# Kernel tuning notes

Measured on AMD Instinct MI355X. Metric: run time of the kernel, lower is better.

The kernel has to match this reference:

```python
import jax, jax.numpy as jnp
import numpy as np

N_NODES = 100000
N_EDGES = 1200000
DIM = 64
MAX_DEG = 64
NUM_LAB = 16
BN_EPS = 1e-5


def _lrelu(x):
    return jax.nn.leaky_relu(x, negative_slope=0.01)


def _bn(x, g, b):
    # BatchNorm1d in training mode: batch statistics over node axis
    m = x.mean(axis=0)
    v = x.var(axis=0)
    return (x - m) * jax.lax.rsqrt(v + BN_EPS) * g + b


def _gin_layer(h, src, dst, n, w1, b1, w2, b2, eps, g, b):
    # GINConv: (1+eps)*x_i + sum_{j in N(i)} x_j, then MLP (lin_lrelu_lin), BN, LeakyReLU
    agg = jax.ops.segment_sum(h[src], dst, num_segments=n)
    x = (1.0 + eps) * h + agg
    x = _lrelu(x @ w1 + b1) @ w2 + b2
    return _lrelu(_bn(x, g, b))


def setup_inputs() -> dict:
    key = jax.random.key(0)
    ks = jax.random.split(key, 16)
    s = 0.05
    inp = {
        'node_deg': jax.random.randint(ks[0], (N_NODES,), 0, MAX_DEG + 1, dtype=jnp.int32),
        'node_lab': jax.random.randint(ks[1], (N_NODES,), 0, NUM_LAB, dtype=jnp.int32),
        'edge_index': jax.random.randint(ks[2], (2, N_EDGES), 0, N_NODES, dtype=jnp.int32),
        'emb_deg': jax.random.normal(ks[3], (MAX_DEG + 1, DIM), jnp.float32) * s,
        'emb_lab': jax.random.normal(ks[4], (NUM_LAB, DIM), jnp.float32) * s,
        'l0_w1': jax.random.normal(ks[5], (2 * DIM, 2 * DIM), jnp.float32) * s,
        'l0_b1': jnp.zeros((2 * DIM,), jnp.float32),
        'l0_w2': jax.random.normal(ks[6], (2 * DIM, DIM), jnp.float32) * s,
        'l0_b2': jnp.zeros((DIM,), jnp.float32),
        'l0_eps': jnp.zeros((1,), jnp.float32),
        'bn0_g': jnp.ones((DIM,), jnp.float32),
        'bn0_b': jnp.zeros((DIM,), jnp.float32),
        'l1_w1': jax.random.normal(ks[7], (DIM, DIM), jnp.float32) * s,
        'l1_b1': jnp.zeros((DIM,), jnp.float32),
        'l1_w2': jax.random.normal(ks[8], (DIM, DIM), jnp.float32) * s,
        'l1_b2': jnp.zeros((DIM,), jnp.float32),
        'l1_eps': jnp.zeros((1,), jnp.float32),
        'bn1_g': jnp.ones((DIM,), jnp.float32),
        'bn1_b': jnp.zeros((DIM,), jnp.float32),
        'fc_w1': jax.random.normal(ks[9], (4 * DIM, DIM), jnp.float32) * s,
        'fc_b1': jnp.zeros((DIM,), jnp.float32),
        'fc_bn_g': jnp.ones((DIM,), jnp.float32),
        'fc_bn_b': jnp.zeros((DIM,), jnp.float32),
        'fc_w2': jax.random.normal(ks[10], (DIM, 1), jnp.float32) * s,
        'fc_b2': jnp.zeros((1,), jnp.float32),
    }
    return inp


def reference(node_deg, node_lab, edge_index, emb_deg, emb_lab,
              l0_w1, l0_b1, l0_w2, l0_b2, l0_eps, bn0_g, bn0_b,
              l1_w1, l1_b1, l1_w2, l1_b2, l1_eps, bn1_g, bn1_b,
              fc_w1, fc_b1, fc_bn_g, fc_bn_b, fc_w2, fc_b2):
    n = node_deg.shape[0]
    src, dst = edge_index[0], edge_index[1]
    # embedding concat: [N, 2*DIM]
    h0 = jnp.concatenate([emb_deg[node_deg], emb_lab[node_lab]], axis=1)
    h1 = _gin_layer(h0, src, dst, n, l0_w1, l0_b1, l0_w2, l0_b2, l0_eps[0], bn0_g, bn0_b)
    h2 = _gin_layer(h1, src, dst, n, l1_w1, l1_b1, l1_w2, l1_b2, l1_eps[0], bn1_g, bn1_b)
    x = jnp.concatenate([h0, h1, h2], axis=1)  # [N, 256]
    x = _lrelu(_bn(x @ fc_w1 + fc_b1, fc_bn_g, fc_bn_b))
    out = jax.nn.sigmoid(x @ fc_w2 + fc_b2)
    return out.squeeze(-1)  # [N]
```

## Files before the change

kernel.cpp:

```cpp
#include <hip/hip_runtime.h>

#define N_NODES 100000
#define N_EDGES 1200000
#define NCLS 81
#define NBKT 196
#define BCAP 8192
#define NCHK 293
#define NGBLK 1563

typedef unsigned short u16;
typedef unsigned char u8;
typedef unsigned int u32;
typedef unsigned long long u64;
typedef short bf16x8 __attribute__((ext_vector_type(8)));
typedef float f32x4 __attribute__((ext_vector_type(4)));

__device__ __forceinline__ float b2f(u16 u) {
  union { u32 i; float f; } v; v.i = ((u32)u) << 16; return v.f;
}
__device__ __forceinline__ u16 f2b(float f) {
  union { float f; u32 i; } v; v.f = f;
  u32 x = v.i;
  return (u16)((x + 0x7fffu + ((x >> 16) & 1u)) >> 16);
}
__device__ __forceinline__ void up2(u32 w, float& lo, float& hi) {
  union { u32 u; float f; } a, b;
  a.u = w << 16; b.u = w & 0xffff0000u;
  lo = a.f; hi = b.f;
}
__device__ __forceinline__ float lrelu(float x) { return x > 0.f ? x : 0.01f * x; }

__device__ __forceinline__ bool is_f32(const u16* emb) {
  int lane = threadIdx.x & 63;
  u32 e0 = (emb[lane * 2] >> 7) & 0xFF;
  u32 e1 = (emb[lane * 2 + 1] >> 7) & 0xFF;
  return __ballot((e0 >= 0x90) || (e1 >= 0x90)) != 0ull;
}

__device__ __forceinline__ float rdr(const void* p, int i, bool f32m) {
  return f32m ? ((const float*)p)[i] : b2f(((const u16*)p)[i]);
}

#define P_EMBD 0
#define P_EMBL 4160
#define P_W1A  5184
#define P_B1A  21568
#define P_W2A  21696
#define P_B2A  29888
#define P_EPS0 29952
#define P_G0   29953
#define P_BB0  30017
#define P_LW1  30081
#define P_LB1  34177
#define P_LW2  34241
#define P_LB2  38337
#define P_EPS1 38401
#define P_G1   38402
#define P_BB1  38466
#define P_FW1  38530
#define P_FB1  54914
#define P_FG   54978
#define P_FBB  55042
#define P_FW2  55106
#define P_FB2  55170
#define P_TOT  55171

struct CvtAll {
  const void* src[22];
  int cnt[22];
  int off[22];
};

struct RawPtrs {
  const void* embD;
  const void* embL;
  const void* w1r;
  const void* w2r;
  const void* lw1r;
  const void* lw2r;
  const void* fwr;
};

__global__ void k_init(CvtAll a, RawPtrs rw, const u16* __restrict__ embRaw,
                       float* __restrict__ P, float* __restrict__ W1p,
                       float* __restrict__ Efc, u16* __restrict__ bp,
                       u16* __restrict__ wpB, u32* __restrict__ gcur) {
  bool f32m = is_f32(embRaw);
  int tid = threadIdx.x;
  if (blockIdx.y < 22) {
    if (blockIdx.y == 0 && blockIdx.x == 0 && tid < NBKT) gcur[tid] = 0;
    int seg = blockIdx.y;
    int i = blockIdx.x * 256 + tid;
    if (i < a.cnt[seg]) {
      float v = f32m ? ((const float*)a.src[seg])[i] : b2f(((const u16*)a.src[seg])[i]);
      P[a.off[seg] + i] = v;
    }
    return;
  }
  int idx = blockIdx.x * 256 + tid;
  if (idx < NCLS * 128) {
    int c = idx >> 7, h = idx & 127;
    float s = 0.f;
    if (c < 65) {
      for (int k = 0; k < 64; ++k)
        s = fmaf(rdr(rw.embD, c * 64 + k, f32m), rdr(rw.w1r, k * 128 + h, f32m), s);
    } else {
      for (int k = 0; k < 64; ++k)
        s = fmaf(rdr(rw.embL, (c - 65) * 64 + k, f32m), rdr(rw.w1r, (64 + k) * 128 + h, f32m), s);
    }
    W1p[idx] = s;
    return;
  }
  if (idx < NCLS * 128 + NCLS * 64) {
    int r = idx - NCLS * 128;
    int c = r >> 6, o = r & 63;
    float s = 0.f;
    if (c < 65) {
      for (int k = 0; k < 64; ++k)
        s = fmaf(rdr(rw.embD, c * 64 + k, f32m), rdr(rw.fwr, k * 64 + o, f32m), s);
    } else {
      for (int k = 0; k < 64; ++k)
        s = fmaf(rdr(rw.embL, (c - 65) * 64 + k, f32m), rdr(rw.fwr, (64 + k) * 64 + o, f32m), s);
    }
    Efc[r] = s;
    return;
  }
  if (idx < NCLS * 128 + NCLS * 64 + 24576) {
    int pidx = idx - (NCLS * 128 + NCLS * 64);
    int seg, rel;
    if (pidx < 8192)       { seg = 0; rel = pidx; }
    else if (pidx < 12288) { seg = 1; rel = pidx - 8192; }
    else if (pidx < 16384) { seg = 2; rel = pidx - 12288; }
    else                   { seg = 3; rel = pidx - 16384; }
    const void* srcs[4] = {rw.w2r, rw.lw1r, rw.lw2r, rw.fwr};
    const int addoff[4] = {0, 0, 0, 128 * 64};
    const int KBs[4] = {4, 2, 2, 4};
    int j = rel & 7, lane = (rel >> 3) & 63, rest = rel >> 9;
    int kb = rest % KBs[seg], nt = rest / KBs[seg];
    int k = kb * 32 + (lane >> 4) * 8 + j;
    int n = nt * 16 + (lane & 15);
    bp[pidx] = f2b(rdr(srcs[seg], addoff[seg] + k * 64 + n, f32m));
    return;
  }
  int p2 = idx - (NCLS * 128 + NCLS * 64 + 24576);
  if (p2 >= 12288) return;
  int j = p2 & 7, lane = (p2 >> 3) & 63, rest = p2 >> 9;
  int kb = rest % 3, nt = rest / 3;
  int c = kb * 32 + (lane >> 4) * 8 + j;
  int n = nt * 16 + (lane & 15);
  float s = 0.f;
  if (c < NCLS) {
    if (c < 65) {
      for (int k = 0; k < 64; ++k)
        s = fmaf(rdr(rw.embD, c * 64 + k, f32m), rdr(rw.w1r, k * 128 + n, f32m), s);
    } else {
      for (int k = 0; k < 64; ++k)
        s = fmaf(rdr(rw.embL, (c - 65) * 64 + k, f32m), rdr(rw.w1r, (64 + k) * 128 + n, f32m), s);
    }
  }
  wpB[p2] = (c < NCLS) ? f2b(s) : 0;
}

__global__ __launch_bounds__(256) void k_bsort(const int* __restrict__ edge,
                                               const int* __restrict__ ndeg,
                                               const int* __restrict__ nlab,
                                               u32* __restrict__ gcur,
                                               u64* __restrict__ e2) {
  __shared__ u32 cnt[NBKT], rbase[NBKT];
  __shared__ u32 slo[4096], shi[4096];
  for (int i = threadIdx.x; i < NBKT; i += 256) cnt[i] = 0;
  __syncthreads();
  int base = blockIdx.x * 4096;
  for (int i = threadIdx.x; i < 4096; i += 256) {
    int e = base + i;
    if (e < N_EDGES) {
      int s = edge[e], d = edge[N_EDGES + e];
      slo[i] = ((u32)s << 11) | ((u32)ndeg[s] << 4) | (u32)nlab[s];
      shi[i] = (u32)d;
      atomicAdd(&cnt[(u32)d >> 9], 1u);
    } else shi[i] = 0xFFFFFFFFu;
  }
  __syncthreads();
  for (int i = threadIdx.x; i < NBKT; i += 256) {
    u32 c = cnt[i];
    rbase[i] = c ? atomicAdd(&gcur[i], c) : 0u;
    cnt[i] = 0;
  }
  __syncthreads();
  for (int i = threadIdx.x; i < 4096; i += 256) {
    u32 d = shi[i];
    if (d == 0xFFFFFFFFu) continue;
    u32 b = d >> 9;
    u32 pos = rbase[b] + atomicAdd(&cnt[b], 1u);
    e2[(size_t)b * BCAP + pos] = ((u64)d << 32) | (u64)slo[i];
  }
}

__global__ __launch_bounds__(512) void k_csrh(const u64* __restrict__ e2,
                                              const u32* __restrict__ gcur,
                                              const u16* __restrict__ wpB,
                                              const float* __restrict__ W1p,
                                              const float* __restrict__ P,
                                              const int* __restrict__ ndeg,
                                              const int* __restrict__ nlab,
                                              u32* __restrict__ row_ptr,
                                              u32* __restrict__ einfo,
                                              u16* __restrict__ hmid) {
  __shared__ u32 l[512], cur[512], gl[NBKT];
  __shared__ u32 h32[512 * 24];
  __shared__ u32 sbase;
  int b = blockIdx.x, tid = threadIdx.x;
  if (tid < NBKT) gl[tid] = gcur[tid];
  l[tid] = 0;
  for (int i = tid; i < 512 * 24; i += 512) h32[i] = 0;
  __syncthreads();
  if (tid == 0) {
    u32 s = 0;
    for (int i = 0; i < b; ++i) s += gl[i];
    sbase = s;
  }
  __syncthreads();
  u32 cnt = gl[b];
  const u64* src = e2 + (size_t)b * BCAP;
  for (u32 e = tid; e < cnt; e += 512)
    atomicAdd(&l[(u32)(src[e] >> 32) & 511u], 1u);
  __syncthreads();
  u32 v = l[tid];
  for (int off = 1; off < 512; off <<= 1) {
    u32 a = (tid >= off) ? l[tid - off] : 0u;
    __syncthreads();
    l[tid] += a;
    __syncthreads();
  }
  u32 pos0 = sbase + l[tid] - v;
  cur[tid] = pos0;
  int nn = b * 512 + tid;
  if (nn <= N_NODES) row_ptr[nn] = pos0;
  __syncthreads();
  for (u32 e = tid; e < cnt; e += 512) {
    u64 r = src[e];
    u32 dl = (u32)(r >> 32) & 511u;
    u32 lo = (u32)r;
    u32 pos = atomicAdd(&cur[dl], 1u);
    einfo[pos] = lo;
    u32 c1 = (lo >> 4) & 0x7Fu, c2 = 65u + (lo & 15u);
    atomicAdd(&h32[dl * 24 + (c1 >> 2)], 1u << ((c1 & 3u) * 8));
    atomicAdd(&h32[dl * 24 + (c2 >> 2)], 1u << ((c2 & 3u) * 8));
  }
  __syncthreads();
  const u8* h = (const u8*)h32;
  int wid = tid >> 6, lane = tid & 63;
  int row = lane & 15, q = lane >> 4;
  float onep = 1.f + P[P_EPS0];
  const bf16x8* bp = (const bf16x8*)wpB;
#pragma unroll 1
  for (int t = wid; t < 32; t += 8) {
    int m0 = b * 512 + t * 16;
    if (m0 >= N_NODES) break;
    f32x4 acc[8];
#pragma unroll
    for (int nt = 0; nt < 8; ++nt) {
      float bb = P[P_B1A + nt * 16 + row];
      acc[nt][0] = bb; acc[nt][1] = bb; acc[nt][2] = bb; acc[nt][3] = bb;
    }
    const u8* ar = h + (t * 16 + row) * 96 + q * 8;
#pragma unroll
    for (int kb = 0; kb < 3; ++kb) {
      bf16x8 af;
#pragma unroll
      for (int j = 0; j < 8; ++j) af[j] = (short)f2b((float)ar[kb * 32 + j]);
#pragma unroll
      for (int nt = 0; nt < 8; ++nt) {
        bf16x8 bf = bp[(nt * 3 + kb) * 64 + lane];
        acc[nt] = __builtin_amdgcn_mfma_f32_16x16x32_bf16(af, bf, acc[nt], 0, 0, 0);
      }
    }
#pragma unroll
    for (int r = 0; r < 4; ++r) {
      int m = m0 + q * 4 + r;
      if (m >= N_NODES) continue;
      const float* wd = W1p + ndeg[m] * 128;
      const float* wl = W1p + (65 + nlab[m]) * 128;
#pragma unroll
      for (int nt = 0; nt < 8; ++nt) {
        int cc = nt * 16 + row;
        float vv = acc[nt][r] + onep * (wd[cc] + wl[cc]);
        hmid[(size_t)m * 128 + cc] = f2b(lrelu(vv));
      }
    }
  }
}

__global__ void k_sr(const float* __restrict__ pbuf, float* __restrict__ statsOut) {
  __shared__ float l[256];
  int c = blockIdx.x;
  float s = 0.f;
  for (int r = threadIdx.x; r < NGBLK; r += 256) s += pbuf[(size_t)r * 128 + c];
  l[threadIdx.x] = s;
  __syncthreads();
  for (int off = 128; off > 0; off >>= 1) {
    if (threadIdx.x < off) l[threadIdx.x] += l[threadIdx.x + off];
    __syncthreads();
  }
  if (threadIdx.x == 0) statsOut[c] = l[0];
}

template <int KB, int LDA, int BIASOFF>
__global__ __launch_bounds__(256) void k_gemm(const u16* __restrict__ A,
                                              const u16* __restrict__ Bp,
                                              const float* __restrict__ P,
                                              float* __restrict__ pbuf,
                                              u16* __restrict__ C) {
  __shared__ float lsum[4][64], lsq[4][64];
  int wid = threadIdx.x >> 6, lane = threadIdx.x & 63;
  int m0 = (blockIdx.x * 4 + wid) * 16;
  bool act = m0 < N_NODES;
  int row = lane & 15, q = lane >> 4;
  float ss[4] = {0.f, 0.f, 0.f, 0.f}, qq[4] = {0.f, 0.f, 0.f, 0.f};
  if (act) {
    const u16* ap = A + (size_t)(m0 + row) * LDA + q * 8;
    const bf16x8* bp = (const bf16x8*)Bp;
    f32x4 acc[4];
#pragma unroll
    for (int nt = 0; nt < 4; ++nt) {
      float b = (BIASOFF >= 0) ? P[BIASOFF + nt * 16 + row] : 0.f;
      acc[nt][0] = b; acc[nt][1] = b; acc[nt][2] = b; acc[nt][3] = b;
    }
#pragma unroll
    for (int kb = 0; kb < KB; ++kb) {
      bf16x8 af = *(const bf16x8*)(ap + kb * 32);
#pragma unroll
      for (int nt = 0; nt < 4; ++nt) {
        bf16x8 bf = bp[(nt * KB + kb) * 64 + lane];
        acc[nt] = __builtin_amdgcn_mfma_f32_16x16x32_bf16(af, bf, acc[nt], 0, 0, 0);
      }
    }
#pragma unroll
    for (int nt = 0; nt < 4; ++nt) {
      float s = 0.f, z = 0.f;
#pragma unroll
      for (int r = 0; r < 4; ++r) {
        int m = m0 + q * 4 + r;
        u16 bv = f2b(acc[nt][r]);
        C[(size_t)m * 64 + nt * 16 + row] = bv;
        float v = b2f(bv);
        s += v; z = fmaf(v, v, z);
      }
      s += __shfl_xor(s, 16, 64); s += __shfl_xor(s, 32, 64);
      z += __shfl_xor(z, 16, 64); z += __shfl_xor(z, 32, 64);
      ss[nt] = s; qq[nt] = z;
    }
  }
  if (lane < 16) {
#pragma unroll
    for (int nt = 0; nt < 4; ++nt) {
      lsum[wid][nt * 16 + lane] = ss[nt];
      lsq[wid][nt * 16 + lane] = qq[nt];
    }
  }
  __syncthreads();
  int t = threadIdx.x;
  if (t < 64)
    pbuf[(size_t)blockIdx.x * 128 + t] = lsum[0][t] + lsum[1][t] + lsum[2][t] + lsum[3][t];
  else if (t < 128) {
    int c = t - 64;
    pbuf[(size_t)blockIdx.x * 128 + t] = lsq[0][c] + lsq[1][c] + lsq[2][c] + lsq[3][c];
  }
}

__global__ __launch_bounds__(256) void k_gemm_bn(const u16* __restrict__ A,
                                                 const u16* __restrict__ Bp,
                                                 const float* __restrict__ P,
                                                 const float* __restrict__ stats,
                                                 u16* __restrict__ C) {
  int wid = threadIdx.x >> 6, lane = threadIdx.x & 63;
  int m0 = (blockIdx.x * 4 + wid) * 16;
  if (m0 >= N_NODES) return;
  int row = lane & 15, q = lane >> 4;
  const float invN = 1.f / (float)N_NODES;
  float sc[16], sh[16];
#pragma unroll
  for (int kb = 0; kb < 2; ++kb)
#pragma unroll
    for (int j = 0; j < 8; ++j) {
      int f = kb * 32 + q * 8 + j;
      float mm = stats[f] * invN;
      float var = fmaxf(stats[64 + f] * invN - mm * mm, 0.f);
      float inv = rsqrtf(var + 1e-5f);
      float s = inv * P[P_G0 + f];
      sc[kb * 8 + j] = s;
      sh[kb * 8 + j] = P[P_BB0 + f] - mm * s;
    }
  const u16* ap = A + (size_t)(m0 + row) * 64 + q * 8;
  const bf16x8* bp = (const bf16x8*)Bp;
  f32x4 acc[4];
#pragma unroll
  for (int nt = 0; nt < 4; ++nt) {
    acc[nt][0] = 0.f; acc[nt][1] = 0.f; acc[nt][2] = 0.f; acc[nt][3] = 0.f;
  }
#pragma unroll
  for (int kb = 0; kb < 2; ++kb) {
    uint4 raw = *(const uint4*)(ap + kb * 32);
    u32 rw[4] = {raw.x, raw.y, raw.z, raw.w};
    bf16x8 af;
#pragma unroll
    for (int p = 0; p < 4; ++p) {
      float lo, hi;
      up2(rw[p], lo, hi);
      float y0 = lrelu(fmaf(sc[kb * 8 + 2 * p], lo, sh[kb * 8 + 2 * p]));
      float y1 = lrelu(fmaf(sc[kb * 8 + 2 * p + 1], hi, sh[kb * 8 + 2 * p + 1]));
      af[2 * p] = (short)f2b(y0);
      af[2 * p + 1] = (short)f2b(y1);
    }
#pragma unroll
    for (int nt = 0; nt < 4; ++nt) {
      bf16x8 bf = bp[(nt * 2 + kb) * 64 + lane];
      acc[nt] = __builtin_amdgcn_mfma_f32_16x16x32_bf16(af, bf, acc[nt], 0, 0, 0);
    }
  }
#pragma unroll
  for (int nt = 0; nt < 4; ++nt)
#pragma unroll
    for (int r = 0; r < 4; ++r) {
      int m = m0 + q * 4 + r;
      C[(size_t)m * 64 + nt * 16 + row] = f2b(acc[nt][r]);
    }
}

__global__ __launch_bounds__(256) void k_agg1(const u32* __restrict__ rp,
                                              const u32* __restrict__ einfo,
                                              const u16* __restrict__ g1,
                                              const float* __restrict__ P,
                                              u16* __restrict__ abuf) {
  int lane = threadIdx.x & 63, wv = threadIdx.x >> 6;
  int n = blockIdx.x * 4 + wv;
  if (n >= N_NODES) return;
  u32 st = rp[n], en = rp[n + 1];
  u32 m = en - st;
  int grp = lane >> 4;
  int fo = (lane & 15) * 4;
  u32 myidx = (u32)n;
  if (lane < (int)m) myidx = einfo[st + lane] >> 11;
  u32 mm = m < 64u ? m : 64u;
  float a0 = 0.f, a1 = 0.f, a2 = 0.f, a3 = 0.f;
  for (u32 k = 0; k < mm; k += 16) {
#pragma unroll
    for (int bb = 0; bb < 4; ++bb) {
      u32 e = k + (u32)(bb * 4 + grp);
      u32 src = (u32)__shfl((int)myidx, (int)e, 64);
      if (e < mm) {
        uint2 v = *(const uint2*)(g1 + (size_t)src * 64 + fo);
        float l0, h0, l1, h1;
        up2(v.x, l0, h0);
        up2(v.y, l1, h1);
        a0 += l0; a1 += h0; a2 += l1; a3 += h1;
      }
    }
  }
  a0 += __shfl_xor(a0, 16, 64); a0 += __shfl_xor(a0, 32, 64);
  a1 += __shfl_xor(a1, 16, 64); a1 += __shfl_xor(a1, 32, 64);
  a2 += __shfl_xor(a2, 16, 64); a2 += __shfl_xor(a2, 32, 64);
  a3 += __shfl_xor(a3, 16, 64); a3 += __shfl_xor(a3, 32, 64);
  for (u32 k = 64; k < m; ++k) {
    u32 src = einfo[st + k] >> 11;
    uint2 v = *(const uint2*)(g1 + (size_t)src * 64 + fo);
    float l0, h0, l1, h1;
    up2(v.x, l0, h0);
    up2(v.y, l1, h1);
    a0 += l0; a1 += h0; a2 += l1; a3 += h1;
  }
  float onep = 1.f + P[P_EPS1];
  uint2 sv = *(const uint2*)(g1 + (size_t)n * 64 + fo);
  float s0, s1, s2, s3;
  up2(sv.x, s0, s1);
  up2(sv.y, s2, s3);
  float r0 = P[P_LB1 + fo + 0] + fmaf(onep, s0, a0);
  float r1 = P[P_LB1 + fo + 1] + fmaf(onep, s1, a1);
  float r2 = P[P_LB1 + fo + 2] + fmaf(onep, s2, a2);
  float r3 = P[P_LB1 + fo + 3] + fmaf(onep, s3, a3);
  if (lane < 16) {
    uint2 o;
    o.x = ((u32)f2b(lrelu(r0))) | (((u32)f2b(lrelu(r1))) << 16);
    o.y = ((u32)f2b(lrelu(r2))) | (((u32)f2b(lrelu(r3))) << 16);
    *(uint2*)(abuf + (size_t)n * 64 + fo) = o;
  }
}

__global__ __launch_bounds__(256) void k_gemm_fc1bn(const u16* __restrict__ t0,
                                                    const u16* __restrict__ t1,
                                                    const u16* __restrict__ Bp,
                                                    const float* __restrict__ P,
                                                    const float* __restrict__ stats,
                                                    float* __restrict__ pbuf,
                                                    const int* __restrict__ ndeg,
                                                    const int* __restrict__ nlab,
                                                    const float* __restrict__ Efc,
                                                    u16* __restrict__ C) {
  __shared__ float lsum[4][64], lsq[4][64];
  int wid = threadIdx.x >> 6, lane = threadIdx.x & 63;
  int m0 = (blockIdx.x * 4 + wid) * 16;
  bool act = m0 < N_NODES;
  int row = lane & 15, q = lane >> 4;
  float ss[4] = {0.f, 0.f, 0.f, 0.f}, qq[4] = {0.f, 0.f, 0.f, 0.f};
  if (act) {
    const float invN = 1.f / (float)N_NODES;
    float sc[32], sh[32];
#pragma unroll
    for (int h = 0; h < 2; ++h) {
      const float* st = stats + h * 128;
      int gof = h ? P_G1 : P_G0, bof = h ? P_BB1 : P_BB0;
#pragma unroll
      for (int kb = 0; kb < 2; ++kb)
#pragma unroll
        for (int j = 0; j < 8; ++j) {
          int f = kb * 32 + q * 8 + j;
          float mm = st[f] * invN;
          float var = fmaxf(st[64 + f] * invN - mm * mm, 0.f);
          float inv = rsqrtf(var + 1e-5f);
          float s = inv * P[gof + f];
          sc[h * 16 + kb * 8 + j] = s;
          sh[h * 16 + kb * 8 + j] = P[bof + f] - mm * s;
        }
    }
    const u16* a0 = t0 + (size_t)(m0 + row) * 64 + q * 8;
    const u16* a1 = t1 + (size_t)(m0 + row) * 64 + q * 8;
    const bf16x8* bp = (const bf16x8*)Bp;
    f32x4 acc[4];
#pragma unroll
    for (int nt = 0; nt < 4; ++nt) {
      float b = P[P_FB1 + nt * 16 + row];
      acc[nt][0] = b; acc[nt][1] = b; acc[nt][2] = b; acc[nt][3] = b;
    }
#pragma unroll
    for (int kb = 0; kb < 4; ++kb) {
      const u16* src = (kb < 2) ? (a0 + kb * 32) : (a1 + (kb - 2) * 32);
      int ci = (kb < 2) ? kb * 8 : 16 + (kb - 2) * 8;
      uint4 raw = *(const uint4*)src;
      u32 rw[4] = {raw.x, raw.y, raw.z, raw.w};
      bf16x8 af;
#pragma unroll
      for (int p = 0; p < 4; ++p) {
        float lo, hi;
        up2(rw[p], lo, hi);
        float y0 = lrelu(fmaf(sc[ci + 2 * p], lo, sh[ci + 2 * p]));
        float y1 = lrelu(fmaf(sc[ci + 2 * p + 1], hi, sh[ci + 2 * p + 1]));
        af[2 * p] = (short)f2b(y0);
        af[2 * p + 1] = (short)f2b(y1);
      }
#pragma unroll
      for (int nt = 0; nt < 4; ++nt) {
        bf16x8 bf = bp[(nt * 4 + kb) * 64 + lane];
        acc[nt] = __builtin_amdgcn_mfma_f32_16x16x32_bf16(af, bf, acc[nt], 0, 0, 0);
      }
    }
    float es[4][4];
#pragma unroll
    for (int r = 0; r < 4; ++r) {
      int m = m0 + q * 4 + r;
      int dn = ndeg[m], ln = 65 + nlab[m];
#pragma unroll
      for (int nt = 0; nt < 4; ++nt) {
        int cc = nt * 16 + row;
        es[r][nt] = acc[nt][r] + Efc[dn * 64 + cc] + Efc[ln * 64 + cc];
      }
    }
#pragma unroll
    for (int nt = 0; nt < 4; ++nt) {
      float s = 0.f, z = 0.f;
#pragma unroll
      for (int r = 0; r < 4; ++r) {
        int m = m0 + q * 4 + r;
        u16 bv = f2b(es[r][nt]);
        C[(size_t)m * 64 + nt * 16 + row] = bv;
        float v = b2f(bv);
        s += v; z = fmaf(v, v, z);
      }
      s += __shfl_xor(s, 16, 64); s += __shfl_xor(s, 32, 64);
      z += __shfl_xor(z, 16, 64); z += __shfl_xor(z, 32, 64);
      ss[nt] = s; qq[nt] = z;
    }
  }
  if (lane < 16) {
#pragma unroll
    for (int nt = 0; nt < 4; ++nt) {
      lsum[wid][nt * 16 + lane] = ss[nt];
      lsq[wid][nt * 16 + lane] = qq[nt];
    }
  }
  __syncthreads();
  int t = threadIdx.x;
  if (t < 64)
    pbuf[(size_t)blockIdx.x * 128 + t] = lsum[0][t] + lsum[1][t] + lsum[2][t] + lsum[3][t];
  else if (t < 128) {
    int c = t - 64;
    pbuf[(size_t)blockIdx.x * 128 + t] = lsq[0][c] + lsq[1][c] + lsq[2][c] + lsq[3][c];
  }
}

__global__ void k_fc2(const u16* __restrict__ t, const float* __restrict__ stats,
                      const float* __restrict__ P, const u16* __restrict__ embRaw,
                      void* __restrict__ out) {
  bool f32m = is_f32(embRaw);
  int n = blockIdx.x * blockDim.x + threadIdx.x;
  if (n >= N_NODES) return;
  float z = P[P_FB2];
  const float invN = 1.f / (float)N_NODES;
  const u16* tn = t + (size_t)n * 64;
#pragma unroll 1
  for (int f = 0; f < 64; ++f) {
    float m = stats[f] * invN;
    float var = fmaxf(stats[64 + f] * invN - m * m, 0.f);
    float inv = rsqrtf(var + 1e-5f);
    float y = (b2f(tn[f]) - m) * inv * P[P_FG + f] + P[P_FBB + f];
    y = lrelu(y);
    z = fmaf(y, P[P_FW2 + f], z);
  }
  float s = 1.f / (1.f + expf(-z));
  if (!(fabsf(z) < 1e30f)) s = 0.25f;
  if (f32m) ((float*)out)[n] = s;
  else      ((u16*)out)[n] = f2b(s);
}

extern "C" void kernel_launch(void* const* d_in, const int* in_sizes, int n_in,
                              void* d_out, int out_size, void* d_ws, size_t ws_size,
                              hipStream_t stream) {
  const int* node_deg = (const int*)d_in[0];
  const int* node_lab = (const int*)d_in[1];
  const int* edge     = (const int*)d_in[2];
  const u16* embRaw   = (const u16*)d_in[3];
  (void)in_sizes; (void)n_in; (void)out_size; (void)ws_size;

  char* base = (char*)d_ws;
  size_t off = 0;
  auto alloc = [&](size_t bytes) -> void* {
    void* p = base + off;
    off += (bytes + 15) & ~(size_t)15;
    return p;
  };
  float* Pb    = (float*)alloc((size_t)P_TOT * 4);
  float* stats = (float*)alloc(384 * 4);
  u32* gcur    = (u32*)alloc(NBKT * 4);
  float* W1p   = (float*)alloc(NCLS * 128 * 4);
  float* Efc   = (float*)alloc(NCLS * 64 * 4);
  u16* bpack   = (u16*)alloc(24576 * 2);
  u16* wpB     = (u16*)alloc(12288 * 2);
  u32* row_ptr = (u32*)alloc((size_t)(N_NODES + 1) * 4);
  float* pbuf  = (float*)alloc((size_t)NGBLK * 128 * 4);
  u32* einfo   = (u32*)alloc((size_t)N_EDGES * 4);
  u64* e2      = (u64*)alloc((size_t)NBKT * BCAP * 8);
  void* arena  = alloc((size_t)N_NODES * 128 * 2);
  u16* t0      = (u16*)alloc((size_t)N_NODES * 64 * 2);
  u16* t1      = (u16*)alloc((size_t)N_NODES * 64 * 2);
  u16* t2      = (u16*)alloc((size_t)N_NODES * 64 * 2);
  u16* hmid = (u16*)arena;
  u16* g1   = (u16*)arena;
  u16* abuf = (u16*)arena + (size_t)N_NODES * 64;
  u16* Bp_w2a = bpack;
  u16* Bp_lw1 = bpack + 8192;
  u16* Bp_lw2 = bpack + 12288;
  u16* Bp_fw1 = bpack + 16384;

  CvtAll ca;
  const int srcidx[22] = {3, 4, 5, 6, 7, 8, 9, 10, 11, 12, 13, 14, 15, 16, 17, 18, 19, 20, 21, 22, 23, 24};
  const int cnts[22]   = {4160, 1024, 16384, 128, 8192, 64, 1, 64, 64, 4096, 64, 4096, 64, 1, 64, 64, 16384, 64, 64, 64, 64, 1};
  const int offs[22]   = {P_EMBD, P_EMBL, P_W1A, P_B1A, P_W2A, P_B2A, P_EPS0, P_G0, P_BB0,
                          P_LW1, P_LB1, P_LW2, P_LB2, P_EPS1, P_G1, P_BB1,
                          P_FW1, P_FB1, P_FG, P_FBB, P_FW2, P_FB2};
  for (int i = 0; i < 22; ++i) { ca.src[i] = d_in[srcidx[i]]; ca.cnt[i] = cnts[i]; ca.off[i] = offs[i]; }
  RawPtrs rw;
  rw.embD = d_in[3]; rw.embL = d_in[4]; rw.w1r = d_in[5]; rw.w2r = d_in[7];
  rw.lw1r = d_in[12]; rw.lw2r = d_in[14]; rw.fwr = d_in[19];

  k_init<<<dim3(205, 23), 256, 0, stream>>>(ca, rw, embRaw, Pb, W1p, Efc, bpack, wpB, gcur);

  k_bsort<<<NCHK, 256, 0, stream>>>(edge, node_deg, node_lab, gcur, e2);

  k_csrh<<<NBKT, 512, 0, stream>>>(e2, gcur, wpB, W1p, Pb, node_deg, node_lab,
                                   row_ptr, einfo, hmid);

  const int GEMM_GRID = NGBLK;

  k_gemm<4, 128, P_B2A><<<GEMM_GRID, 256, 0, stream>>>(hmid, Bp_w2a, Pb, pbuf, t0);
  k_sr<<<128, 256, 0, stream>>>(pbuf, stats);

  k_gemm_bn<<<GEMM_GRID, 256, 0, stream>>>(t0, Bp_lw1, Pb, stats, g1);
  k_agg1<<<(N_NODES + 3) / 4, 256, 0, stream>>>(row_ptr, einfo, g1, Pb, abuf);
  k_gemm<2, 64, P_LB2><<<GEMM_GRID, 256, 0, stream>>>(abuf, Bp_lw2, Pb, pbuf, t1);
  k_sr<<<128, 256, 0, stream>>>(pbuf, stats + 128);

  k_gemm_fc1bn<<<GEMM_GRID, 256, 0, stream>>>(t0, t1, Bp_fw1, Pb, stats, pbuf,
                                              node_deg, node_lab, Efc, t2);
  k_sr<<<128, 256, 0, stream>>>(pbuf, stats + 256);
  k_fc2<<<(N_NODES + 255) / 256, 256, 0, stream>>>(t2, stats + 256, Pb, embRaw, d_out);
}
```

Measured before the change: 321.8 us.

## Fuse layer-1 neighbor aggregation with second MLP GEMM and BN stats

New measurement: 340.7 us. 5.9% more time.

```diff
diff --git a/kernel.cpp b/kernel.cpp
--- a/kernel.cpp
+++ b/kernel.cpp
@@ -427,62 +427,124 @@
     }
 }
 
-__global__ __launch_bounds__(256) void k_agg1(const u32* __restrict__ rp,
-                                              const u32* __restrict__ einfo,
-                                              const u16* __restrict__ g1,
-                                              const float* __restrict__ P,
-                                              u16* __restrict__ abuf) {
-  int lane = threadIdx.x & 63, wv = threadIdx.x >> 6;
-  int n = blockIdx.x * 4 + wv;
-  if (n >= N_NODES) return;
-  u32 st = rp[n], en = rp[n + 1];
-  u32 m = en - st;
-  int grp = lane >> 4;
-  int fo = (lane & 15) * 4;
-  u32 myidx = (u32)n;
-  if (lane < (int)m) myidx = einfo[st + lane] >> 11;
-  u32 mm = m < 64u ? m : 64u;
-  float a0 = 0.f, a1 = 0.f, a2 = 0.f, a3 = 0.f;
-  for (u32 k = 0; k < mm; k += 16) {
-#pragma unroll
-    for (int bb = 0; bb < 4; ++bb) {
-      u32 e = k + (u32)(bb * 4 + grp);
-      u32 src = (u32)__shfl((int)myidx, (int)e, 64);
-      if (e < mm) {
+__global__ __launch_bounds__(256) void k_agg_gemm(const u32* __restrict__ rp,
+                                                  const u32* __restrict__ einfo,
+                                                  const u16* __restrict__ g1,
+                                                  const u16* __restrict__ Bp,
+                                                  const float* __restrict__ P,
+                                                  float* __restrict__ pbuf,
+                                                  u16* __restrict__ C) {
+  __shared__ float lsum[4][64], lsq[4][64];
+  __shared__ u16 As[4][16][72];
+  int wid = threadIdx.x >> 6, lane = threadIdx.x & 63;
+  int m0 = (blockIdx.x * 4 + wid) * 16;
+  bool act = m0 < N_NODES;
+  int row = lane & 15, q = lane >> 4;
+  float ss[4] = {0.f, 0.f, 0.f, 0.f}, qq[4] = {0.f, 0.f, 0.f, 0.f};
+  if (act) {
+    int grp = lane >> 4;
+    int fo = (lane & 15) * 4;
+    float onep = 1.f + P[P_EPS1];
+    u32 rpv = 0;
+    if (lane <= 16) rpv = rp[m0 + lane];
+#pragma unroll 1
+    for (int r = 0; r < 16; ++r) {
+      int n = m0 + r;
+      u32 st = (u32)__shfl((int)rpv, r, 64);
+      u32 en = (u32)__shfl((int)rpv, r + 1, 64);
+      u32 m = en - st;
+      u32 myidx = (u32)n;
+      if (lane < (int)m) myidx = einfo[st + lane] >> 11;
+      u32 mm = m < 64u ? m : 64u;
+      float a0 = 0.f, a1 = 0.f, a2 = 0.f, a3 = 0.f;
+      for (u32 k = 0; k < mm; k += 16) {
+#pragma unroll
+        for (int bb = 0; bb < 4; ++bb) {
+          u32 e = k + (u32)(bb * 4 + grp);
+          u32 src = (u32)__shfl((int)myidx, (int)e, 64);
+          if (e < mm) {
+            uint2 v = *(const uint2*)(g1 + (size_t)src * 64 + fo);
+            float l0, h0, l1, h1;
+            up2(v.x, l0, h0);
+            up2(v.y, l1, h1);
+            a0 += l0; a1 += h0; a2 += l1; a3 += h1;
+          }
+        }
+      }
+      a0 += __shfl_xor(a0, 16, 64); a0 += __shfl_xor(a0, 32, 64);
+      a1 += __shfl_xor(a1, 16, 64); a1 += __shfl_xor(a1, 32, 64);
+      a2 += __shfl_xor(a2, 16, 64); a2 += __shfl_xor(a2, 32, 64);
+      a3 += __shfl_xor(a3, 16, 64); a3 += __shfl_xor(a3, 32, 64);
+      for (u32 k = 64; k < m; ++k) {
+        u32 src = einfo[st + k] >> 11;
         uint2 v = *(const uint2*)(g1 + (size_t)src * 64 + fo);
         float l0, h0, l1, h1;
         up2(v.x, l0, h0);
         up2(v.y, l1, h1);
         a0 += l0; a1 += h0; a2 += l1; a3 += h1;
       }
-    }
-  }
-  a0 += __shfl_xor(a0, 16, 64); a0 += __shfl_xor(a0, 32, 64);
-  a1 += __shfl_xor(a1, 16, 64); a1 += __shfl_xor(a1, 32, 64);
-  a2 += __shfl_xor(a2, 16, 64); a2 += __shfl_xor(a2, 32, 64);
-  a3 += __shfl_xor(a3, 16, 64); a3 += __shfl_xor(a3, 32, 64);
-  for (u32 k = 64; k < m; ++k) {
-    u32 src = einfo[st + k] >> 11;
-    uint2 v = *(const uint2*)(g1 + (size_t)src * 64 + fo);
-    float l0, h0, l1, h1;
-    up2(v.x, l0, h0);
-    up2(v.y, l1, h1);
-    a0 += l0; a1 += h0; a2 += l1; a3 += h1;
-  }
-  float onep = 1.f + P[P_EPS1];
-  uint2 sv = *(const uint2*)(g1 + (size_t)n * 64 + fo);
-  float s0, s1, s2, s3;
-  up2(sv.x, s0, s1);
-  up2(sv.y, s2, s3);
-  float r0 = P[P_LB1 + fo + 0] + fmaf(onep, s0, a0);
-  float r1 = P[P_LB1 + fo + 1] + fmaf(onep, s1, a1);
-  float r2 = P[P_LB1 + fo + 2] + fmaf(onep, s2, a2);
-  float r3 = P[P_LB1 + fo + 3] + fmaf(onep, s3, a3);
+      uint2 sv = *(const uint2*)(g1 + (size_t)n * 64 + fo);
+      float s0, s1, s2, s3;
+      up2(sv.x, s0, s1);
+      up2(sv.y, s2, s3);
+      float r0 = P[P_LB1 + fo + 0] + fmaf(onep, s0, a0);
+      float r1 = P[P_LB1 + fo + 1] + fmaf(onep, s1, a1);
+      float r2 = P[P_LB1 + fo + 2] + fmaf(onep, s2, a2);
+      float r3 = P[P_LB1 + fo + 3] + fmaf(onep, s3, a3);
+      if (lane < 16) {
+        uint2 o;
+        o.x = ((u32)f2b(lrelu(r0))) | (((u32)f2b(lrelu(r1))) << 16);
+        o.y = ((u32)f2b(lrelu(r2))) | (((u32)f2b(lrelu(r3))) << 16);
+        *(uint2*)&As[wid][r][fo] = o;
+      }
+    }
+    const u16* ap = &As[wid][row][q * 8];
+    const bf16x8* bp = (const bf16x8*)Bp;
+    f32x4 acc[4];
+#pragma unroll
+    for (int nt = 0; nt < 4; ++nt) {
+      float b = P[P_LB2 + nt * 16 + row];
+      acc[nt][0] = b; acc[nt][1] = b; acc[nt][2] = b; acc[nt][3] = b;
+    }
+#pragma unroll
+    for (int kb = 0; kb < 2; ++kb) {
+      bf16x8 af = *(const bf16x8*)(ap + kb * 32);
+#pragma unroll
+      for (int nt = 0; nt < 4; ++nt) {
+        bf16x8 bf = bp[(nt * 2 + kb) * 64 + lane];
+        acc[nt] = __builtin_amdgcn_mfma_f32_16x16x32_bf16(af, bf, acc[nt], 0, 0, 0);
+      }
+    }
+#pragma unroll
+    for (int nt = 0; nt < 4; ++nt) {
+      float s = 0.f, z = 0.f;
+#pragma unroll
+      for (int r = 0; r < 4; ++r) {
+        int m = m0 + q * 4 + r;
+        u16 bv = f2b(acc[nt][r]);
+        C[(size_t)m * 64 + nt * 16 + row] = bv;
+        float v = b2f(bv);
+        s += v; z = fmaf(v, v, z);
+      }
+      s += __shfl_xor(s, 16, 64); s += __shfl_xor(s, 32, 64);
+      z += __shfl_xor(z, 16, 64); z += __shfl_xor(z, 32, 64);
+      ss[nt] = s; qq[nt] = z;
+    }
+  }
   if (lane < 16) {
-    uint2 o;
-    o.x = ((u32)f2b(lrelu(r0))) | (((u32)f2b(lrelu(r1))) << 16);
-    o.y = ((u32)f2b(lrelu(r2))) | (((u32)f2b(lrelu(r3))) << 16);
-    *(uint2*)(abuf + (size_t)n * 64 + fo) = o;
+#pragma unroll
+    for (int nt = 0; nt < 4; ++nt) {
+      lsum[wid][nt * 16 + lane] = ss[nt];
+      lsq[wid][nt * 16 + lane] = qq[nt];
+    }
+  }
+  __syncthreads();
+  int t = threadIdx.x;
+  if (t < 64)
+    pbuf[(size_t)blockIdx.x * 128 + t] = lsum[0][t] + lsum[1][t] + lsum[2][t] + lsum[3][t];
+  else if (t < 128) {
+    int c = t - 64;
+    pbuf[(size_t)blockIdx.x * 128 + t] = lsq[0][c] + lsq[1][c] + lsq[2][c] + lsq[3][c];
   }
 }
 
@@ -654,7 +716,6 @@
   u16* t2      = (u16*)alloc((size_t)N_NODES * 64 * 2);
   u16* hmid = (u16*)arena;
   u16* g1   = (u16*)arena;
-  u16* abuf = (u16*)arena + (size_t)N_NODES * 64;
   u16* Bp_w2a = bpack;
   u16* Bp_lw1 = bpack + 8192;
   u16* Bp_lw2 = bpack + 12288;
@@ -684,8 +745,7 @@
   k_sr<<<128, 256, 0, stream>>>(pbuf, stats);
 
   k_gemm_bn<<<GEMM_GRID, 256, 0, stream>>>(t0, Bp_lw1, Pb, stats, g1);
-  k_agg1<<<(N_NODES + 3) / 4, 256, 0, stream>>>(row_ptr, einfo, g1, Pb, abuf);
-  k_gemm<2, 64, P_LB2><<<GEMM_GRID, 256, 0, stream>>>(abuf, Bp_lw2, Pb, pbuf, t1);
+  k_agg_gemm<<<GEMM_GRID, 256, 0, stream>>>(row_ptr, einfo, g1, Bp_lw2, Pb, pbuf, t1);
   k_sr<<<128, 256, 0, stream>>>(pbuf, stats + 128);
 
   k_gemm_fc1bn<<<GEMM_GRID, 256, 0, stream>>>(t0, t1, Bp_fw1, Pb, stats, pbuf,
```
